# Optimization experiments

Hardware: AMD Instinct MI355X
Metric: run time of the kernel (lower is better)

## Reference

```python
import jax, jax.numpy as jnp
import numpy as np

TAU = 1.0
BASE = 7
NUM_TWISTS = 3
EPS = 1e-6

B, S, D, P, M = 4, 2048, 1024, 9, 256


def _rot(y, theta):
    # learned rotation in the (0,1) channel plane; theta broadcasts against y[..., 0]
    c, s = jnp.cos(theta), jnp.sin(theta)
    y0, y1 = y[..., 0], y[..., 1]
    r0 = (y0 * c - y1 * s)[..., None]
    r1 = (y0 * s + y1 * c)[..., None]
    return jnp.concatenate([r0, r1, y[..., 2:]], axis=-1)


def _mod_phase_norm(x, g, base=BASE):
    # RMS-normalize within channel groups defined by (channel index mod base)
    d = x.shape[-1]
    gid = jnp.arange(d) % base
    oh = jax.nn.one_hot(gid, base, dtype=x.dtype)           # [d, base]
    cnt = oh.sum(axis=0)                                    # [base]
    msq = (x * x) @ oh / cnt                                # [..., base]
    denom = jnp.sqrt(jnp.take(msq, gid, axis=-1) + EPS)     # [..., d]
    return x / denom * g


def setup_inputs() -> dict:
    key = jax.random.key(0)
    ks = jax.random.split(key, 16)
    w = lambda k, shape, scale: jax.random.normal(k, shape, dtype=jnp.float32) * scale
    u = jax.random.uniform(ks[1], (NUM_TWISTS + 1, B, S, P), dtype=jnp.float32,
                           minval=1e-6, maxval=1.0 - 1e-6)
    gumbel_noise = -jnp.log(-jnp.log(u))
    return {
        'x': w(ks[0], (B, S, D), 1.0),
        'gumbel_noise': gumbel_noise,
        'mixer_w': w(ks[2], (3, D), 0.5),
        'obs_W1': w(ks[3], (2 * D, M), (2 * D) ** -0.5),
        'obs_b1': jnp.zeros((M,), jnp.float32),
        'obs_th1': w(ks[4], (), 0.1),
        'obs_W2': w(ks[5], (M, P), M ** -0.5),
        'obs_b2': jnp.zeros((P,), jnp.float32),
        'obs_th2': w(ks[6], (), 0.1),
        'path_Wa': w(ks[7], (P, D, M), D ** -0.5),
        'path_ba': jnp.zeros((P, M), jnp.float32),
        'path_tha': w(ks[8], (P,), 0.1),
        'path_Wb': w(ks[9], (P, M, D), M ** -0.5),
        'path_bb': jnp.zeros((P, D), jnp.float32),
        'path_thb': w(ks[10], (P,), 0.1),
        'twist_W': w(ks[11], (D, D), D ** -0.5),
        'twist_b': jnp.zeros((D,), jnp.float32),
        'twist_th': w(ks[12], (), 0.1),
        'norm_g': jnp.ones((D,), jnp.float32),
    }


def reference(x, gumbel_noise, mixer_w, obs_W1, obs_b1, obs_th1, obs_W2, obs_b2,
              obs_th2, path_Wa, path_ba, path_tha, path_Wb, path_bb, path_thb,
              twist_W, twist_b, twist_th, norm_g):
    # neighbor mixer: per-channel 3-tap mix over sequence (zero-padded, non-causal)
    xp = jnp.pad(x, ((0, 0), (1, 1), (0, 0)))
    x_mixed = x * mixer_w[0] + xp[:, :-2] * mixer_w[1] + xp[:, 2:] * mixer_w[2]

    def observer_logits(collapsed):
        combined = jnp.concatenate([x_mixed, collapsed], axis=-1)      # [B,S,2D]
        h = jnp.tanh(_rot(combined @ obs_W1 + obs_b1, obs_th1))        # [B,S,M]
        return _rot(h @ obs_W2 + obs_b2, obs_th2)                      # [B,S,P]

    def path_outputs_fn(tin):
        h = _rot(jnp.einsum('bsd,pdm->bspm', tin, path_Wa) + path_ba, path_tha)
        return _rot(jnp.einsum('bspm,pmd->bspd', h, path_Wb) + path_bb, path_thb)

    collapsed = jnp.zeros_like(x_mixed)
    path_out = None
    for t in range(NUM_TWISTS):
        logits = observer_logits(collapsed)
        rw = jax.nn.softmax((logits + gumbel_noise[t]) / TAU, axis=-1)  # soft gumbel
        tin = x_mixed + _rot(collapsed @ twist_W + twist_b, twist_th)
        path_out = path_outputs_fn(tin)                                # [B,S,P,D]
        collapsed = _mod_phase_norm(jnp.einsum('bspd,bsp->bsd', path_out, rw), norm_g)

    # final hard (straight-through) gumbel routing, reusing last path_out
    final_logits = observer_logits(collapsed)
    soft = jax.nn.softmax((final_logits + gumbel_noise[NUM_TWISTS]) / TAU, axis=-1)
    hard = jax.nn.one_hot(jnp.argmax(soft, axis=-1), P, dtype=soft.dtype)
    rw_hard = hard + soft - jax.lax.stop_gradient(soft)
    final_collapsed = jnp.einsum('bspd,bsp->bsd', path_out, rw_hard)

    # dropout is identity in eval mode
    out = _mod_phase_norm(x + final_collapsed, norm_g)
    collapsed = _mod_phase_norm(collapsed, norm_g)
    return out, collapsed
```

## Files before the change

kernel.cpp:

```cpp
#include <hip/hip_runtime.h>
#include <hip/hip_bf16.h>

typedef unsigned short u16;
typedef short bf16x8 __attribute__((ext_vector_type(8)));
typedef float f32x4 __attribute__((ext_vector_type(4)));

constexpr int Dd = 1024, Pp = 9, Mm = 256, Nn = 8192, Kc = 2304;
constexpr float EPSf = 1e-6f;

__device__ __forceinline__ float bf2f(u16 u) {
    union { unsigned int u; float f; } v; v.u = ((unsigned int)u) << 16; return v.f;
}
__device__ __forceinline__ u16 f2bf(float f) {
    union { float f; unsigned int u; } v; v.f = f;
    unsigned int r = (v.u + 0x7FFFu + ((v.u >> 16) & 1u)) >> 16; return (u16)r;
}
__device__ __forceinline__ void split2(float v, u16& h, u16& l) {
    h = f2bf(v); l = f2bf(v - bf2f(h));
}
__device__ __forceinline__ void gld16(u16* lds, const u16* g) {
    __builtin_amdgcn_global_load_lds(
        (const __attribute__((address_space(1))) unsigned int*)g,
        (__attribute__((address_space(3))) unsigned int*)lds, 16, 0, 0);
}

__global__ void rotcopy_k(const float* __restrict__ src, float* __restrict__ dst,
                          int R, int C, const float* __restrict__ theta, int Pb)
{
    long total = (long)Pb * R * C;
    long idx = (long)blockIdx.x * 256 + threadIdx.x;
    if (idx >= total) return;
    int c = (int)(idx % C);
    long rp = idx / C;
    int r = (int)(rp % R);
    int pb = (int)(rp / R);
    float th = theta[pb];
    const float* s = src + ((long)pb * R + r) * C;
    float v;
    if (c == 0)      v = s[0] * cosf(th) - s[1] * sinf(th);
    else if (c == 1) v = s[0] * sinf(th) + s[1] * cosf(th);
    else             v = s[c];
    dst[idx] = v;
}

__global__ void splitW1_k(const float* __restrict__ W1, const float* __restrict__ th,
                          u16* __restrict__ h, u16* __restrict__ l)
{
    int idx = blockIdx.x * 256 + threadIdx.x;
    if (idx >= 256 * 2048) return;
    int k = idx & 2047, n = idx >> 11;
    float v;
    if (n == 0)      v = W1[(long)k * 256 + 0] * cosf(th[0]) - W1[(long)k * 256 + 1] * sinf(th[0]);
    else if (n == 1) v = W1[(long)k * 256 + 0] * sinf(th[0]) + W1[(long)k * 256 + 1] * cosf(th[0]);
    else             v = W1[(long)k * 256 + n];
    u16 hh, ll; split2(v, hh, ll); h[idx] = hh; l[idx] = ll;
}

__global__ void splitTW_k(const float* __restrict__ tW, const float* __restrict__ th,
                          u16* __restrict__ h, u16* __restrict__ l)
{
    int idx = blockIdx.x * 256 + threadIdx.x;
    if (idx >= 1024 * 1024) return;
    int k = idx & 1023, n = idx >> 10;
    float v;
    if (n == 0)      v = tW[(long)k * 1024 + 0] * cosf(th[0]) - tW[(long)k * 1024 + 1] * sinf(th[0]);
    else if (n == 1) v = tW[(long)k * 1024 + 0] * sinf(th[0]) + tW[(long)k * 1024 + 1] * cosf(th[0]);
    else             v = tW[(long)k * 1024 + n];
    u16 hh, ll; split2(v, hh, ll); h[idx] = hh; l[idx] = ll;
}

__global__ void splitWa_k(const float* __restrict__ Wa, const float* __restrict__ tha,
                          u16* __restrict__ h, u16* __restrict__ l)
{
    int idx = blockIdx.x * 256 + threadIdx.x;
    if (idx >= Kc * 1024) return;
    int k = idx & 1023, n = idx >> 10;
    int p = n >> 8, m = n & 255;
    const float* s = Wa + ((long)p * 1024 + k) * 256;
    float v;
    if (m == 0)      v = s[0] * cosf(tha[p]) - s[1] * sinf(tha[p]);
    else if (m == 1) v = s[0] * sinf(tha[p]) + s[1] * cosf(tha[p]);
    else             v = s[m];
    u16 hh, ll; split2(v, hh, ll); h[idx] = hh; l[idx] = ll;
}

__global__ void splitWb_k(const float* __restrict__ Wb, const float* __restrict__ thb,
                          u16* __restrict__ h, u16* __restrict__ l)
{
    int idx = blockIdx.x * 256 + threadIdx.x;
    if (idx >= 1024 * Kc) return;
    int n = idx / Kc;
    int k = idx - n * Kc;
    int p = k >> 8, m = k & 255;
    const float* s = Wb + ((long)p * 256 + m) * 1024;
    float v;
    if (n == 0)      v = s[0] * cosf(thb[p]) - s[1] * sinf(thb[p]);
    else if (n == 1) v = s[0] * sinf(thb[p]) + s[1] * cosf(thb[p]);
    else             v = s[n];
    u16 hh, ll; split2(v, hh, ll); h[idx] = hh; l[idx] = ll;
}

__global__ void mixer_k(const float* __restrict__ x, const float* __restrict__ mw,
                        u16* __restrict__ xmh, u16* __restrict__ xml)
{
    int idx = blockIdx.x * 256 + threadIdx.x;
    if (idx >= Nn * Dd / 4) return;
    int d4 = idx & (Dd / 4 - 1);
    int n = idx >> 8;
    int s = n & 2047;
    const float4* x4 = (const float4*)x;
    const float4* w4 = (const float4*)mw;
    float4 xc = x4[idx];
    float4 w0 = w4[d4], w1 = w4[(Dd / 4) + d4], w2 = w4[2 * (Dd / 4) + d4];
    float o[4];
    o[0] = xc.x * w0.x; o[1] = xc.y * w0.y; o[2] = xc.z * w0.z; o[3] = xc.w * w0.w;
    if (s > 0) {
        float4 xl = x4[idx - Dd / 4];
        o[0] += xl.x * w1.x; o[1] += xl.y * w1.y; o[2] += xl.z * w1.z; o[3] += xl.w * w1.w;
    }
    if (s < 2047) {
        float4 xr = x4[idx + Dd / 4];
        o[0] += xr.x * w2.x; o[1] += xr.y * w2.y; o[2] += xr.z * w2.z; o[3] += xr.w * w2.w;
    }
    ushort4 h4, l4;
    split2(o[0], h4.x, l4.x); split2(o[1], h4.y, l4.y);
    split2(o[2], h4.z, l4.z); split2(o[3], h4.w, l4.w);
    ((ushort4*)xmh)[idx] = h4; ((ushort4*)xml)[idx] = l4;
}

__global__ void tanh_k(const float* __restrict__ a, float* __restrict__ o, int total)
{
    int idx = blockIdx.x * 256 + threadIdx.x;
    if (idx < total) o[idx] = tanhf(a[idx]);
}

__global__ void addb_split_k(const u16* __restrict__ xmh, const u16* __restrict__ xml,
                             const float* __restrict__ tbr,
                             u16* __restrict__ th_, u16* __restrict__ tl_)
{
    int idx = blockIdx.x * 256 + threadIdx.x;
    if (idx >= Nn * Dd / 4) return;
    int d4 = idx & (Dd / 4 - 1);
    ushort4 xh = ((const ushort4*)xmh)[idx], xl = ((const ushort4*)xml)[idx];
    float4 b = ((const float4*)tbr)[d4];
    ushort4 h4, l4;
    split2(bf2f(xh.x) + bf2f(xl.x) + b.x, h4.x, l4.x);
    split2(bf2f(xh.y) + bf2f(xl.y) + b.y, h4.y, l4.y);
    split2(bf2f(xh.z) + bf2f(xl.z) + b.z, h4.z, l4.z);
    split2(bf2f(xh.w) + bf2f(xl.w) + b.w, h4.w, l4.w);
    ((ushort4*)th_)[idx] = h4; ((ushort4*)tl_)[idx] = l4;
}

template<int EPI>
__global__ __launch_bounds__(256, 2) void mgemm(
    const u16* __restrict__ Agh, const u16* __restrict__ Agl, int lda,
    const u16* __restrict__ Bgh, const u16* __restrict__ Bgl, int ldb,
    int K,
    float* __restrict__ Cf, u16* __restrict__ Coh, u16* __restrict__ Col, int ldc,
    const float* __restrict__ Cinit,
    const u16* __restrict__ CIh, const u16* __restrict__ CIl,
    const float* __restrict__ bias,
    const float* __restrict__ rwv,
    const float* __restrict__ rwv2,
    const float* __restrict__ bbrv)
{
    __shared__ u16 smem[2][16384];
    const int tid = threadIdx.x, wave = tid >> 6, lane = tid & 63;
    const int nwg = gridDim.x * gridDim.y;
    const int flat = blockIdx.y * gridDim.x + blockIdx.x;
    const int q = nwg >> 3;
    const int l_ = (flat & 7) * q + (flat >> 3);
    const int r0 = (l_ / gridDim.x) * 128, c0 = (l_ % gridDim.x) * 128;
    const int srl = lane >> 2;
    const int ssl = ((lane & 3) ^ ((lane >> 3) & 3)) * 8;
    const int frl = lane & 15, kh = lane >> 4;
    const int sw  = (kh ^ ((frl >> 1) & 3)) * 8;
    const int arow0 = (wave >> 1) * 64, bcol0 = (wave & 1) * 64;
    const int w32 = wave * 32;

    f32x4 acc[4][4] = {};
    f32x4 acc2[4][4];
    if constexpr (EPI == 4) {
#pragma unroll
        for (int i = 0; i < 4; ++i)
#pragma unroll
            for (int j = 0; j < 4; ++j) acc2[i][j] = f32x4{0.f, 0.f, 0.f, 0.f};
    }

    auto STAGE = [&](int buf, int k0) {
        u16* base = &smem[buf][0];
        u16* As_h = base;        u16* As_l = base + 4096;
        u16* Bs_h = base + 8192; u16* Bs_l = base + 12288;
        const long ga0 = (long)(r0 + w32 + srl) * lda + k0 + ssl;
        gld16(&As_h[w32 * 32],        Agh + ga0);
        gld16(&As_h[(w32 + 16) * 32], Agh + ga0 + 16L * lda);
        gld16(&As_l[w32 * 32],        Agl + ga0);
        gld16(&As_l[(w32 + 16) * 32], Agl + ga0 + 16L * lda);
        const long gb0 = (long)(c0 + w32 + srl) * ldb + k0 + ssl;
        gld16(&Bs_h[w32 * 32],        Bgh + gb0);
        gld16(&Bs_h[(w32 + 16) * 32], Bgh + gb0 + 16L * ldb);
        gld16(&Bs_l[w32 * 32],        Bgl + gb0);
        gld16(&Bs_l[(w32 + 16) * 32], Bgl + gb0 + 16L * ldb);
    };
    auto COMPUTE = [&](int buf, f32x4 (&ac)[4][4]) {
        u16* base = &smem[buf][0];
        u16* As_h = base;        u16* As_l = base + 4096;
        u16* Bs_h = base + 8192; u16* Bs_l = base + 12288;
        bf16x8 ah[4], al[4];
#pragma unroll
        for (int f = 0; f < 4; ++f) {
            int ao = (arow0 + f * 16 + frl) * 32 + sw;
            ah[f] = *(const bf16x8*)&As_h[ao];
            al[f] = *(const bf16x8*)&As_l[ao];
        }
#pragma unroll
        for (int j = 0; j < 4; ++j) {
            int bo = (bcol0 + j * 16 + frl) * 32 + sw;
            bf16x8 bh = *(const bf16x8*)&Bs_h[bo];
            bf16x8 bl = *(const bf16x8*)&Bs_l[bo];
#pragma unroll
            for (int i = 0; i < 4; ++i) {
                ac[i][j] = __builtin_amdgcn_mfma_f32_16x16x32_bf16(ah[i], bh, ac[i][j], 0, 0, 0);
                ac[i][j] = __builtin_amdgcn_mfma_f32_16x16x32_bf16(ah[i], bl, ac[i][j], 0, 0, 0);
                ac[i][j] = __builtin_amdgcn_mfma_f32_16x16x32_bf16(al[i], bh, ac[i][j], 0, 0, 0);
            }
        }
    };
    auto FLUSH = [&](int p) {
#pragma unroll
        for (int i = 0; i < 4; ++i)
#pragma unroll
            for (int reg = 0; reg < 4; ++reg) {
                float w = rwv[(long)(r0 + arow0 + i * 16 + kh * 4 + reg) * 9 + p];
#pragma unroll
                for (int j = 0; j < 4; ++j) {
                    acc[i][j][reg] += w * acc2[i][j][reg];
                    acc2[i][j][reg] = 0.f;
                }
            }
    };

    const int NT = K / 32;
    STAGE(0, 0);
#pragma unroll 1
    for (int t = 0; t < NT; t += 2) {
        STAGE(1, (t + 1) * 32);
        asm volatile("s_waitcnt vmcnt(8)" ::: "memory");
        __builtin_amdgcn_sched_barrier(0);
        __builtin_amdgcn_s_barrier();
        __builtin_amdgcn_sched_barrier(0);
        if constexpr (EPI == 4) COMPUTE(0, acc2); else COMPUTE(0, acc);
        __builtin_amdgcn_sched_barrier(0);
        __builtin_amdgcn_s_barrier();
        __builtin_amdgcn_sched_barrier(0);
        if (t + 2 < NT) {
            STAGE(0, (t + 2) * 32);
            asm volatile("s_waitcnt vmcnt(8)" ::: "memory");
        } else {
            asm volatile("s_waitcnt vmcnt(0)" ::: "memory");
        }
        __builtin_amdgcn_sched_barrier(0);
        __builtin_amdgcn_s_barrier();
        __builtin_amdgcn_sched_barrier(0);
        if constexpr (EPI == 4) COMPUTE(1, acc2); else COMPUTE(1, acc);
        __builtin_amdgcn_sched_barrier(0);
        __builtin_amdgcn_s_barrier();
        __builtin_amdgcn_sched_barrier(0);
        if constexpr (EPI == 4) {
            if (((t + 1) & 7) == 7) FLUSH((t + 1) >> 3);
        }
    }

#pragma unroll
    for (int i = 0; i < 4; ++i)
#pragma unroll
        for (int reg = 0; reg < 4; ++reg) {
            const int r = r0 + arow0 + i * 16 + kh * 4 + reg;
#pragma unroll
            for (int j = 0; j < 4; ++j) {
                const int c = c0 + bcol0 + j * 16 + frl;
                float v = acc[i][j][reg];
                if constexpr (EPI == 0) {
                    Cf[(long)r * ldc + c] = v + bias[c];
                } else if constexpr (EPI == 1) {
                    Cf[(long)r * ldc + c] = tanhf(v + Cinit[(long)r * ldc + c]);
                } else if constexpr (EPI == 2) {
                    long o = (long)r * ldc + c;
                    v += bf2f(CIh[o]) + bf2f(CIl[o]) + bias[c];
                    u16 h, l; split2(v, h, l); Coh[o] = h; Col[o] = l;
                } else if constexpr (EPI == 3) {
                    long o = (long)r * ldc + c;
                    v = (v + bias[c]) * rwv[(long)r * 9 + (c >> 8)];
                    u16 h, l; split2(v, h, l); Coh[o] = h; Col[o] = l;
                } else if constexpr (EPI == 4) {
#pragma unroll
                    for (int p = 0; p < 9; ++p) v += rwv2[(long)r * 9 + p] * bbrv[p * 1024 + c];
                    Cf[(long)r * ldc + c] = v;
                } else {
#pragma unroll
                    for (int p = 0; p < 9; ++p) v += rwv[(long)r * 9 + p] * bbrv[p * 1024 + c];
                    Cf[(long)r * ldc + c] = v;
                }
            }
        }
}

__global__ void logits_k(const float* __restrict__ h, const float* __restrict__ W2r,
                         const float* __restrict__ b2r, const float* __restrict__ gum,
                         float* __restrict__ rwA, float* __restrict__ rwH,
                         const float* __restrict__ rwS, int hard)
{
    __shared__ float hs[Mm];
    __shared__ float lg[16];
    int n = blockIdx.x;
    for (int i = threadIdx.x; i < Mm; i += 64) hs[i] = h[(long)n * Mm + i];
    __syncthreads();
    if (threadIdx.x < Pp) {
        int p = threadIdx.x;
        float acc = b2r[p];
        for (int m = 0; m < Mm; ++m) acc += hs[m] * W2r[m * Pp + p];
        lg[p] = acc + gum[(long)n * Pp + p];
    }
    __syncthreads();
    if (threadIdx.x == 0) {
        float mx = lg[0]; int am = 0;
#pragma unroll
        for (int p = 1; p < Pp; ++p) if (lg[p] > mx) { mx = lg[p]; am = p; }
        if (hard) {
#pragma unroll
            for (int p = 0; p < Pp; ++p) {
                rwA[(long)n * Pp + p] = (p == am) ? 1.f / rwS[(long)n * Pp + p] : 0.f;
                rwH[(long)n * Pp + p] = (p == am) ? 1.f : 0.f;
            }
        } else {
            float e[Pp]; float ssum = 0.f;
#pragma unroll
            for (int p = 0; p < Pp; ++p) { e[p] = expf(lg[p] - mx); ssum += e[p]; }
#pragma unroll
            for (int p = 0; p < Pp; ++p) rwA[(long)n * Pp + p] = e[p] / ssum;
        }
    }
}

template<int INSPLIT, int OUTSPLIT>
__global__ void norm_k(const float* __restrict__ in,
                       const u16* __restrict__ inh, const u16* __restrict__ inl,
                       const float* __restrict__ add, const float* __restrict__ g,
                       float* __restrict__ outf, u16* __restrict__ oh, u16* __restrict__ ol)
{
    __shared__ float sb[256][8];
    __shared__ float dn[8];
    int n = blockIdx.x;
    int t = threadIdx.x;
    float v[4];
#pragma unroll
    for (int j = 0; j < 7; ++j) sb[t][j] = 0.f;
#pragma unroll
    for (int i = 0; i < 4; ++i) {
        int d = t + i * 256;
        long o = (long)n * Dd + d;
        float xv = INSPLIT ? (bf2f(inh[o]) + bf2f(inl[o])) : in[o];
        if (add) xv += add[o];
        v[i] = xv;
        sb[t][d % 7] += xv * xv;
    }
    __syncthreads();
    for (int st = 128; st >= 1; st >>= 1) {
        if (t < st) {
#pragma unroll
            for (int j = 0; j < 7; ++j) sb[t][j] += sb[t + st][j];
        }
        __syncthreads();
    }
    if (t < 7) {
        const float cnt = (t < 2) ? 147.f : 146.f;
        dn[t] = 1.f / sqrtf(sb[0][t] / cnt + EPSf);
    }
    __syncthreads();
#pragma unroll
    for (int i = 0; i < 4; ++i) {
        int d = t + i * 256;
        long o = (long)n * Dd + d;
        float ov = v[i] * dn[d % 7] * g[d];
        if (OUTSPLIT) { u16 h, l; split2(ov, h, l); oh[o] = h; ol[o] = l; }
        else outf[o] = ov;
    }
}

static inline int cdiv(long a, long b) { return (int)((a + b - 1) / b); }

extern "C" void kernel_launch(void* const* d_in, const int* in_sizes, int n_in,
                              void* d_out, int out_size, void* d_ws, size_t ws_size,
                              hipStream_t stream)
{
    const float* x    = (const float*)d_in[0];
    const float* gum  = (const float*)d_in[1];
    const float* mw   = (const float*)d_in[2];
    const float* W1   = (const float*)d_in[3];
    const float* b1   = (const float*)d_in[4];
    const float* th1  = (const float*)d_in[5];
    const float* W2   = (const float*)d_in[6];
    const float* b2   = (const float*)d_in[7];
    const float* th2  = (const float*)d_in[8];
    const float* Wa   = (const float*)d_in[9];
    const float* ba   = (const float*)d_in[10];
    const float* tha  = (const float*)d_in[11];
    const float* Wb   = (const float*)d_in[12];
    const float* bbv  = (const float*)d_in[13];
    const float* thb  = (const float*)d_in[14];
    const float* tW   = (const float*)d_in[15];
    const float* tb   = (const float*)d_in[16];
    const float* tth  = (const float*)d_in[17];
    const float* gnorm = (const float*)d_in[18];

    char* cur = (char*)d_ws;
    auto alloc = [&](size_t bytes) -> void* {
        void* r = (void*)cur; cur += (bytes + 255) & ~(size_t)255; return r;
    };
    void* region = alloc((size_t)Nn * Dd * 4);
    float* craw = (float*)region;
    float* hbuf = (float*)region;
    u16*   tinh = (u16*)region;
    u16*   tinl = tinh + (size_t)Nn * Dd;
    float* zx   = (float*)alloc((size_t)Nn * Mm * 4);
    float* rwS  = (float*)alloc((size_t)Nn * Pp * 4);
    float* rwD  = (float*)alloc((size_t)Nn * Pp * 4);
    float* rwH  = (float*)alloc((size_t)Nn * Pp * 4);
    u16* xmh  = (u16*)alloc((size_t)Nn * Dd * 2);
    u16* xml  = (u16*)alloc((size_t)Nn * Dd * 2);
    u16* colh = (u16*)alloc((size_t)Nn * Dd * 2);
    u16* coll = (u16*)alloc((size_t)Nn * Dd * 2);
    u16* hph  = (u16*)alloc((size_t)Nn * Kc * 2);
    u16* hpl  = (u16*)alloc((size_t)Nn * Kc * 2);
    u16* W1th = (u16*)alloc(256 * 2048 * 2);
    u16* W1tl = (u16*)alloc(256 * 2048 * 2);
    u16* tWth = (u16*)alloc(1024 * 1024 * 2);
    u16* tWtl = (u16*)alloc(1024 * 1024 * 2);
    u16* Wath = (u16*)alloc((size_t)Kc * 1024 * 2);
    u16* Watl = (u16*)alloc((size_t)Kc * 1024 * 2);
    u16* Wbth = (u16*)alloc((size_t)1024 * Kc * 2);
    u16* Wbtl = (u16*)alloc((size_t)1024 * Kc * 2);
    float* W2r = (float*)alloc(256 * 9 * 4);
    float* b1r = (float*)alloc(256 * 4);
    float* b2r = (float*)alloc(16 * 4);
    float* bac = (float*)alloc(Kc * 4);
    float* bbr = (float*)alloc(Pp * 1024 * 4);
    float* tbr = (float*)alloc(1024 * 4);
    if ((size_t)(cur - (char*)d_ws) > ws_size) return;

    float* out0 = (float*)d_out;
    float* out1 = out0 + (long)Nn * Dd;

    splitW1_k<<<2048, 256, 0, stream>>>(W1, th1, W1th, W1tl);
    splitTW_k<<<4096, 256, 0, stream>>>(tW, tth, tWth, tWtl);
    splitWa_k<<<cdiv((long)Kc * 1024, 256), 256, 0, stream>>>(Wa, tha, Wath, Watl);
    splitWb_k<<<cdiv((long)1024 * Kc, 256), 256, 0, stream>>>(Wb, thb, Wbth, Wbtl);
    rotcopy_k<<<cdiv(256L * 9, 256), 256, 0, stream>>>(W2, W2r, 256, 9, th2, 1);
    rotcopy_k<<<1, 256, 0, stream>>>(b1, b1r, 1, 256, th1, 1);
    rotcopy_k<<<1, 256, 0, stream>>>(b2, b2r, 1, 9, th2, 1);
    rotcopy_k<<<cdiv((long)Pp * Mm, 256), 256, 0, stream>>>(ba, bac, 1, 256, tha, 9);
    rotcopy_k<<<cdiv((long)Pp * 1024, 256), 256, 0, stream>>>(bbv, bbr, 1, 1024, thb, 9);
    rotcopy_k<<<cdiv(1024L, 256), 256, 0, stream>>>(tb, tbr, 1, 1024, tth, 1);

    mixer_k<<<Nn * Dd / 4 / 256, 256, 0, stream>>>(x, mw, xmh, xml);

    mgemm<0><<<dim3(2, 64), 256, 0, stream>>>(
        xmh, xml, 1024, W1th, W1tl, 2048, 1024,
        zx, nullptr, nullptr, 256, nullptr, nullptr, nullptr, b1r, nullptr, nullptr, nullptr);

    for (int t = 0; t < 3; ++t) {
        if (t == 0) {
            tanh_k<<<cdiv((long)Nn * Mm, 256), 256, 0, stream>>>(zx, hbuf, Nn * Mm);
        } else {
            mgemm<1><<<dim3(2, 64), 256, 0, stream>>>(
                colh, coll, 1024, W1th + 1024, W1tl + 1024, 2048, 1024,
                hbuf, nullptr, nullptr, 256, zx, nullptr, nullptr, nullptr, nullptr, nullptr, nullptr);
        }
        logits_k<<<Nn, 64, 0, stream>>>(hbuf, W2r, b2r, gum + (long)t * Nn * Pp,
                                        rwS, nullptr, nullptr, 0);
        if (t == 0) {
            addb_split_k<<<Nn * Dd / 4 / 256, 256, 0, stream>>>(xmh, xml, tbr, tinh, tinl);
        } else {
            mgemm<2><<<dim3(8, 64), 256, 0, stream>>>(
                colh, coll, 1024, tWth, tWtl, 1024, 1024,
                nullptr, tinh, tinl, 1024, nullptr, xmh, xml, tbr, nullptr, nullptr, nullptr);
        }
        mgemm<3><<<dim3(18, 64), 256, 0, stream>>>(
            tinh, tinl, 1024, Wath, Watl, 1024, 1024,
            nullptr, hph, hpl, Kc, nullptr, nullptr, nullptr, bac, rwS, nullptr, nullptr);
        mgemm<5><<<dim3(8, 64), 256, 0, stream>>>(
            hph, hpl, Kc, Wbth, Wbtl, Kc, Kc,
            craw, nullptr, nullptr, 1024, nullptr, nullptr, nullptr, nullptr, rwS, nullptr, bbr);
        norm_k<0, 1><<<Nn, 256, 0, stream>>>(craw, nullptr, nullptr, nullptr, gnorm,
                                             nullptr, colh, coll);
    }

    mgemm<1><<<dim3(2, 64), 256, 0, stream>>>(
        colh, coll, 1024, W1th + 1024, W1tl + 1024, 2048, 1024,
        hbuf, nullptr, nullptr, 256, zx, nullptr, nullptr, nullptr, nullptr, nullptr, nullptr);
    logits_k<<<Nn, 64, 0, stream>>>(hbuf, W2r, b2r, gum + 3L * Nn * Pp,
                                    rwD, rwH, rwS, 1);
    mgemm<4><<<dim3(8, 64), 256, 0, stream>>>(
        hph, hpl, Kc, Wbth, Wbtl, Kc, Kc,
        craw, nullptr, nullptr, 1024, nullptr, nullptr, nullptr, nullptr, rwD, rwH, bbr);
    norm_k<0, 0><<<Nn, 256, 0, stream>>>(craw, nullptr, nullptr, x, gnorm, out0, nullptr, nullptr);
    norm_k<1, 0><<<Nn, 256, 0, stream>>>(nullptr, colh, coll, nullptr, gnorm, out1, nullptr, nullptr);
}
```

Measured before the change: 1.434 ms.

## Add 512-thread 256x128 tiled GEMM with register-prefetched B for big GEMMs

Adds a new mgemm2 kernel with 512 threads, a 256x128 output tile per workgroup, and an LDS double buffer for A. B fragments are loaded straight from global memory into registers one K-tile ahead, and MFMA sections run under raised priority. Workgroup ids are remapped so that neighbouring blocks share data in cache. The twist, path-A and path-B GEMMs move to this kernel to get more reuse per workgroup and better overlap of loads with MFMA, at the cost of more registers and fewer workgroups.

```diff
diff --git a/kernel.cpp b/kernel.cpp
--- a/kernel.cpp
+++ b/kernel.cpp
@@ -7,6 +7,8 @@
 
 constexpr int Dd = 1024, Pp = 9, Mm = 256, Nn = 8192, Kc = 2304;
 constexpr float EPSf = 1e-6f;
+
+template<int N> struct ic { static constexpr int v = N; };
 
 __device__ __forceinline__ float bf2f(u16 u) {
     union { unsigned int u; float f; } v; v.u = ((unsigned int)u) << 16; return v.f;
@@ -284,7 +286,113 @@
                     Cf[(long)r * ldc + c] = v + bias[c];
                 } else if constexpr (EPI == 1) {
                     Cf[(long)r * ldc + c] = tanhf(v + Cinit[(long)r * ldc + c]);
-                } else if constexpr (EPI == 2) {
+                } else if constexpr (EPI == 4) {
+#pragma unroll
+                    for (int p = 0; p < 9; ++p) v += rwv2[(long)r * 9 + p] * bbrv[p * 1024 + c];
+                    Cf[(long)r * ldc + c] = v;
+                }
+            }
+        }
+}
+
+template<int EPI>
+__global__ __launch_bounds__(512, 2) void mgemm2(
+    const u16* __restrict__ Agh, const u16* __restrict__ Agl, int lda,
+    const u16* __restrict__ Bgh, const u16* __restrict__ Bgl, int ldb,
+    int K,
+    float* __restrict__ Cf, u16* __restrict__ Coh, u16* __restrict__ Col, int ldc,
+    const u16* __restrict__ CIh, const u16* __restrict__ CIl,
+    const float* __restrict__ bias,
+    const float* __restrict__ rwv,
+    const float* __restrict__ bbrv)
+{
+    __shared__ u16 smem[2][16384];
+    const int tid = threadIdx.x, wave = tid >> 6, lane = tid & 63;
+    const int nwg = gridDim.x * gridDim.y;
+    const int flat = blockIdx.y * gridDim.x + blockIdx.x;
+    const int q = nwg >> 3;
+    const int l_ = (flat & 7) * q + (flat >> 3);
+    const int r0 = (l_ / gridDim.x) * 256, c0 = (l_ % gridDim.x) * 128;
+    const int srl = lane >> 2;
+    const int ssl = ((lane & 3) ^ ((lane >> 3) & 3)) * 8;
+    const int frl = lane & 15, kh = lane >> 4;
+    const int sw  = (kh ^ ((frl >> 1) & 3)) * 8;
+    const int arow0 = (wave >> 1) * 64, bcol0 = (wave & 1) * 64;
+    const int w32 = wave * 32;
+    const int NT = K / 32;
+
+    f32x4 acc[4][4] = {};
+    bf16x8 bA[8], bB[8];
+
+    auto STAGE_A = [&](int buf, int k0) {
+        u16* Ash = &smem[buf][0];
+        u16* Asl = &smem[buf][8192];
+        const long ga = (long)(r0 + w32 + srl) * lda + k0 + ssl;
+        gld16(&Ash[w32 * 32],        Agh + ga);
+        gld16(&Ash[(w32 + 16) * 32], Agh + ga + 16L * lda);
+        gld16(&Asl[w32 * 32],        Agl + ga);
+        gld16(&Asl[(w32 + 16) * 32], Agl + ga + 16L * lda);
+    };
+    auto LOADB1 = [&](bf16x8 (&dst)[8], int j, int k0) {
+        const long gb = (long)(c0 + bcol0 + j * 16 + frl) * ldb + k0 + kh * 8;
+        dst[j * 2]     = *(const bf16x8*)(Bgh + gb);
+        dst[j * 2 + 1] = *(const bf16x8*)(Bgl + gb);
+    };
+
+    auto TILE = [&](auto P, int t, bf16x8 (&bcur)[8], bf16x8 (&bnxt)[8]) {
+        constexpr int par = decltype(P)::v;
+        asm volatile("s_waitcnt vmcnt(0) lgkmcnt(0)" ::: "memory");
+        __builtin_amdgcn_sched_barrier(0);
+        __builtin_amdgcn_s_barrier();
+        __builtin_amdgcn_sched_barrier(0);
+        if (t + 1 < NT) STAGE_A(par ^ 1, (t + 1) * 32);
+        u16* Ash = &smem[par][0];
+        u16* Asl = &smem[par][8192];
+        bf16x8 ah[4], al[4];
+#pragma unroll
+        for (int f = 0; f < 4; ++f) {
+            int ao = (arow0 + f * 16 + frl) * 32 + sw;
+            ah[f] = *(const bf16x8*)&Ash[ao];
+            al[f] = *(const bf16x8*)&Asl[ao];
+        }
+#pragma unroll
+        for (int j = 0; j < 4; ++j) {
+            bf16x8 bh = bcur[j * 2], bl = bcur[j * 2 + 1];
+            __builtin_amdgcn_s_setprio(1);
+#pragma unroll
+            for (int i = 0; i < 4; ++i)
+                acc[i][j] = __builtin_amdgcn_mfma_f32_16x16x32_bf16(ah[i], bh, acc[i][j], 0, 0, 0);
+#pragma unroll
+            for (int i = 0; i < 4; ++i)
+                acc[i][j] = __builtin_amdgcn_mfma_f32_16x16x32_bf16(ah[i], bl, acc[i][j], 0, 0, 0);
+#pragma unroll
+            for (int i = 0; i < 4; ++i)
+                acc[i][j] = __builtin_amdgcn_mfma_f32_16x16x32_bf16(al[i], bh, acc[i][j], 0, 0, 0);
+            __builtin_amdgcn_s_setprio(0);
+            if (t + 1 < NT) LOADB1(bnxt, j, (t + 1) * 32);
+        }
+    };
+
+    STAGE_A(0, 0);
+#pragma unroll
+    for (int j = 0; j < 4; ++j) LOADB1(bA, j, 0);
+
+#pragma unroll 1
+    for (int t = 0; t < NT; t += 2) {
+        TILE(ic<0>{}, t,     bA, bB);
+        TILE(ic<1>{}, t + 1, bB, bA);
+    }
+
+#pragma unroll
+    for (int i = 0; i < 4; ++i)
+#pragma unroll
+        for (int reg = 0; reg < 4; ++reg) {
+            const int r = r0 + arow0 + i * 16 + kh * 4 + reg;
+#pragma unroll
+            for (int j = 0; j < 4; ++j) {
+                const int c = c0 + bcol0 + j * 16 + frl;
+                float v = acc[i][j][reg];
+                if constexpr (EPI == 2) {
                     long o = (long)r * ldc + c;
                     v += bf2f(CIh[o]) + bf2f(CIl[o]) + bias[c];
                     u16 h, l; split2(v, h, l); Coh[o] = h; Col[o] = l;
@@ -292,10 +400,6 @@
                     long o = (long)r * ldc + c;
                     v = (v + bias[c]) * rwv[(long)r * 9 + (c >> 8)];
                     u16 h, l; split2(v, h, l); Coh[o] = h; Col[o] = l;
-                } else if constexpr (EPI == 4) {
-#pragma unroll
-                    for (int p = 0; p < 9; ++p) v += rwv2[(long)r * 9 + p] * bbrv[p * 1024 + c];
-                    Cf[(long)r * ldc + c] = v;
                 } else {
 #pragma unroll
                     for (int p = 0; p < 9; ++p) v += rwv[(long)r * 9 + p] * bbrv[p * 1024 + c];
@@ -481,16 +585,16 @@
         if (t == 0) {
             addb_split_k<<<Nn * Dd / 4 / 256, 256, 0, stream>>>(xmh, xml, tbr, tinh, tinl);
         } else {
-            mgemm<2><<<dim3(8, 64), 256, 0, stream>>>(
+            mgemm2<2><<<dim3(8, 32), 512, 0, stream>>>(
                 colh, coll, 1024, tWth, tWtl, 1024, 1024,
-                nullptr, tinh, tinl, 1024, nullptr, xmh, xml, tbr, nullptr, nullptr, nullptr);
-        }
-        mgemm<3><<<dim3(18, 64), 256, 0, stream>>>(
+                nullptr, tinh, tinl, 1024, xmh, xml, tbr, nullptr, nullptr);
+        }
+        mgemm2<3><<<dim3(18, 32), 512, 0, stream>>>(
             tinh, tinl, 1024, Wath, Watl, 1024, 1024,
-            nullptr, hph, hpl, Kc, nullptr, nullptr, nullptr, bac, rwS, nullptr, nullptr);
-        mgemm<5><<<dim3(8, 64), 256, 0, stream>>>(
+            nullptr, hph, hpl, Kc, nullptr, nullptr, bac, rwS, nullptr);
+        mgemm2<5><<<dim3(8, 32), 512, 0, stream>>>(
             hph, hpl, Kc, Wbth, Wbtl, Kc, Kc,
-            craw, nullptr, nullptr, 1024, nullptr, nullptr, nullptr, nullptr, rwS, nullptr, bbr);
+            craw, nullptr, nullptr, 1024, nullptr, nullptr, nullptr, rwS, bbr);
         norm_k<0, 1><<<Nn, 256, 0, stream>>>(craw, nullptr, nullptr, nullptr, gnorm,
                                              nullptr, colh, coll);
     }
```

Measured after the change: 2.109 ms. 47.1% more time.

## Fold twist matrix into path-A weights to skip per-iteration twist GEMM

Applied to the files above, without the earlier changes.

Precomputes a fused weight (twist_W rotated, times path_Wa) and a fused bias, so each later iteration computes hidden path activations straight from collapsed with one GEMM plus a precomputed x_mixed@Wa term. This removes the 1024x1024 twist GEMM and the tin intermediate per iteration. The first iteration uses an elementwise kernel on the precomputed x_mixed projection. It costs one extra Nn x Kc split buffer and a weight-product GEMM at setup, and falls back to the old path if workspace is too small. Pre-multiplying the weights changes the rounding order of the split-bf16 arithmetic.

```diff
diff --git a/kernel.cpp b/kernel.cpp
--- a/kernel.cpp
+++ b/kernel.cpp
@@ -69,6 +69,20 @@
     u16 hh, ll; split2(v, hh, ll); h[idx] = hh; l[idx] = ll;
 }
 
+__global__ void splitTWT_k(const float* __restrict__ tW, const float* __restrict__ th,
+                           u16* __restrict__ h, u16* __restrict__ l)
+{
+    int idx = blockIdx.x * 256 + threadIdx.x;
+    if (idx >= 1024 * 1024) return;
+    int d = idx & 1023, e = idx >> 10;
+    const float* s = tW + (long)e * 1024;
+    float v;
+    if (d == 0)      v = s[0] * cosf(th[0]) - s[1] * sinf(th[0]);
+    else if (d == 1) v = s[0] * sinf(th[0]) + s[1] * cosf(th[0]);
+    else             v = s[d];
+    u16 hh, ll; split2(v, hh, ll); h[idx] = hh; l[idx] = ll;
+}
+
 __global__ void splitWa_k(const float* __restrict__ Wa, const float* __restrict__ tha,
                           u16* __restrict__ h, u16* __restrict__ l)
 {
@@ -98,6 +112,44 @@
     else if (n == 1) v = s[0] * sinf(thb[p]) + s[1] * cosf(thb[p]);
     else             v = s[n];
     u16 hh, ll; split2(v, hh, ll); h[idx] = hh; l[idx] = ll;
+}
+
+__global__ void bac2_k(const float* __restrict__ bac, const float* __restrict__ tbr,
+                       const u16* __restrict__ Wath, const u16* __restrict__ Watl,
+                       float* __restrict__ bac2)
+{
+    __shared__ float sb[256];
+    int pm = blockIdx.x;
+    int t = threadIdx.x;
+    float s = 0.f;
+    for (int d = t; d < 1024; d += 256) {
+        long o = (long)pm * 1024 + d;
+        s += tbr[d] * (bf2f(Wath[o]) + bf2f(Watl[o]));
+    }
+    sb[t] = s; __syncthreads();
+    for (int st = 128; st >= 1; st >>= 1) {
+        if (t < st) sb[t] += sb[t + st];
+        __syncthreads();
+    }
+    if (t == 0) bac2[pm] = bac[pm] + sb[0];
+}
+
+__global__ void hp0_k(const u16* __restrict__ zxah, const u16* __restrict__ zxal,
+                      const float* __restrict__ rw,
+                      u16* __restrict__ hph, u16* __restrict__ hpl)
+{
+    int idx = blockIdx.x * 256 + threadIdx.x;
+    if (idx >= Nn * Kc / 4) return;
+    int c4 = idx % (Kc / 4);
+    int n  = idx / (Kc / 4);
+    float w = rw[(long)n * Pp + (c4 >> 6)];
+    ushort4 zh = ((const ushort4*)zxah)[idx], zl = ((const ushort4*)zxal)[idx];
+    ushort4 h4, l4;
+    split2((bf2f(zh.x) + bf2f(zl.x)) * w, h4.x, l4.x);
+    split2((bf2f(zh.y) + bf2f(zl.y)) * w, h4.y, l4.y);
+    split2((bf2f(zh.z) + bf2f(zl.z)) * w, h4.z, l4.z);
+    split2((bf2f(zh.w) + bf2f(zl.w)) * w, h4.w, l4.w);
+    ((ushort4*)hph)[idx] = h4; ((ushort4*)hpl)[idx] = l4;
 }
 
 __global__ void mixer_k(const float* __restrict__ x, const float* __restrict__ mw,
@@ -279,27 +331,32 @@
 #pragma unroll
             for (int j = 0; j < 4; ++j) {
                 const int c = c0 + bcol0 + j * 16 + frl;
+                const long o = (long)r * ldc + c;
                 float v = acc[i][j][reg];
                 if constexpr (EPI == 0) {
-                    Cf[(long)r * ldc + c] = v + bias[c];
+                    Cf[o] = v + bias[c];
                 } else if constexpr (EPI == 1) {
-                    Cf[(long)r * ldc + c] = tanhf(v + Cinit[(long)r * ldc + c]);
+                    Cf[o] = tanhf(v + Cinit[o]);
                 } else if constexpr (EPI == 2) {
-                    long o = (long)r * ldc + c;
                     v += bf2f(CIh[o]) + bf2f(CIl[o]) + bias[c];
                     u16 h, l; split2(v, h, l); Coh[o] = h; Col[o] = l;
                 } else if constexpr (EPI == 3) {
-                    long o = (long)r * ldc + c;
                     v = (v + bias[c]) * rwv[(long)r * 9 + (c >> 8)];
                     u16 h, l; split2(v, h, l); Coh[o] = h; Col[o] = l;
                 } else if constexpr (EPI == 4) {
 #pragma unroll
                     for (int p = 0; p < 9; ++p) v += rwv2[(long)r * 9 + p] * bbrv[p * 1024 + c];
-                    Cf[(long)r * ldc + c] = v;
+                    Cf[o] = v;
+                } else if constexpr (EPI == 5) {
+#pragma unroll
+                    for (int p = 0; p < 9; ++p) v += rwv[(long)r * 9 + p] * bbrv[p * 1024 + c];
+                    Cf[o] = v;
+                } else if constexpr (EPI == 6) {
+                    if (bias) v += bias[c];
+                    u16 h, l; split2(v, h, l); Coh[o] = h; Col[o] = l;
                 } else {
-#pragma unroll
-                    for (int p = 0; p < 9; ++p) v += rwv[(long)r * 9 + p] * bbrv[p * 1024 + c];
-                    Cf[(long)r * ldc + c] = v;
+                    v = (v + bf2f(CIh[o]) + bf2f(CIl[o])) * rwv[(long)r * 9 + (c >> 8)];
+                    u16 h, l; split2(v, h, l); Coh[o] = h; Col[o] = l;
                 }
             }
         }
@@ -388,6 +445,7 @@
 }
 
 static inline int cdiv(long a, long b) { return (int)((a + b - 1) / b); }
+static inline size_t al256(size_t b) { return (b + 255) & ~(size_t)255; }
 
 extern "C" void kernel_launch(void* const* d_in, const int* in_sizes, int n_in,
                               void* d_out, int out_size, void* d_ws, size_t ws_size,
@@ -413,46 +471,56 @@
     const float* tth  = (const float*)d_in[17];
     const float* gnorm = (const float*)d_in[18];
 
+    const size_t szRegion = al256((size_t)Nn * Dd * 4);
+    const size_t szZx   = al256((size_t)Nn * Mm * 4);
+    const size_t szRw   = al256((size_t)Nn * Pp * 4);
+    const size_t szColH = al256((size_t)Nn * Dd * 2);
+    const size_t szHpH  = al256((size_t)Nn * Kc * 2);
+    const size_t szW1H  = al256((size_t)256 * 2048 * 2);
+    const size_t szWatH = al256((size_t)Kc * 1024 * 2);
+    const size_t szWbH  = al256((size_t)1024 * Kc * 2);
+    const size_t szTWH  = al256((size_t)1024 * 1024 * 2);
+    const size_t szMisc = al256(256 * 9 * 4) + al256(256 * 4) + al256(64)
+                        + al256(Kc * 4) + al256(Kc * 4) + al256(Pp * 1024 * 4) + al256(1024 * 4);
+    const size_t need_common = szRegion + szZx + 3 * szRw + 2 * szColH + 2 * szHpH
+                             + 2 * szW1H + 2 * szWatH + 2 * szWbH + szMisc;
+    const size_t need_new = 2 * szHpH  + 2 * szTWH  + 2 * szWatH ;
+    const size_t need_old = 2 * szColH  + 2 * szTWH ;
+    const bool NEWP = ws_size >= need_common + need_new;
+    if (!NEWP && ws_size < need_common + need_old) return;
+
     char* cur = (char*)d_ws;
-    auto alloc = [&](size_t bytes) -> void* {
-        void* r = (void*)cur; cur += (bytes + 255) & ~(size_t)255; return r;
-    };
+    auto alloc = [&](size_t bytes) -> void* { void* r = cur; cur += al256(bytes); return r; };
+
     void* region = alloc((size_t)Nn * Dd * 4);
-    float* craw = (float*)region;
-    float* hbuf = (float*)region;
-    u16*   tinh = (u16*)region;
-    u16*   tinl = tinh + (size_t)Nn * Dd;
     float* zx   = (float*)alloc((size_t)Nn * Mm * 4);
     float* rwS  = (float*)alloc((size_t)Nn * Pp * 4);
     float* rwD  = (float*)alloc((size_t)Nn * Pp * 4);
     float* rwH  = (float*)alloc((size_t)Nn * Pp * 4);
-    u16* xmh  = (u16*)alloc((size_t)Nn * Dd * 2);
-    u16* xml  = (u16*)alloc((size_t)Nn * Dd * 2);
     u16* colh = (u16*)alloc((size_t)Nn * Dd * 2);
     u16* coll = (u16*)alloc((size_t)Nn * Dd * 2);
     u16* hph  = (u16*)alloc((size_t)Nn * Kc * 2);
     u16* hpl  = (u16*)alloc((size_t)Nn * Kc * 2);
     u16* W1th = (u16*)alloc(256 * 2048 * 2);
     u16* W1tl = (u16*)alloc(256 * 2048 * 2);
-    u16* tWth = (u16*)alloc(1024 * 1024 * 2);
-    u16* tWtl = (u16*)alloc(1024 * 1024 * 2);
     u16* Wath = (u16*)alloc((size_t)Kc * 1024 * 2);
     u16* Watl = (u16*)alloc((size_t)Kc * 1024 * 2);
     u16* Wbth = (u16*)alloc((size_t)1024 * Kc * 2);
     u16* Wbtl = (u16*)alloc((size_t)1024 * Kc * 2);
-    float* W2r = (float*)alloc(256 * 9 * 4);
-    float* b1r = (float*)alloc(256 * 4);
-    float* b2r = (float*)alloc(16 * 4);
-    float* bac = (float*)alloc(Kc * 4);
-    float* bbr = (float*)alloc(Pp * 1024 * 4);
-    float* tbr = (float*)alloc(1024 * 4);
-    if ((size_t)(cur - (char*)d_ws) > ws_size) return;
-
+    float* W2r  = (float*)alloc(256 * 9 * 4);
+    float* b1r  = (float*)alloc(256 * 4);
+    float* b2r  = (float*)alloc(64);
+    float* bac  = (float*)alloc(Kc * 4);
+    float* bac2 = (float*)alloc(Kc * 4);
+    float* bbr  = (float*)alloc(Pp * 1024 * 4);
+    float* tbr  = (float*)alloc(1024 * 4);
+
+    float* hbuf = (float*)region;
+    float* craw = (float*)region;
     float* out0 = (float*)d_out;
     float* out1 = out0 + (long)Nn * Dd;
 
     splitW1_k<<<2048, 256, 0, stream>>>(W1, th1, W1th, W1tl);
-    splitTW_k<<<4096, 256, 0, stream>>>(tW, tth, tWth, tWtl);
     splitWa_k<<<cdiv((long)Kc * 1024, 256), 256, 0, stream>>>(Wa, tha, Wath, Watl);
     splitWb_k<<<cdiv((long)1024 * Kc, 256), 256, 0, stream>>>(Wb, thb, Wbth, Wbtl);
     rotcopy_k<<<cdiv(256L * 9, 256), 256, 0, stream>>>(W2, W2r, 256, 9, th2, 1);
@@ -462,47 +530,125 @@
     rotcopy_k<<<cdiv((long)Pp * 1024, 256), 256, 0, stream>>>(bbv, bbr, 1, 1024, thb, 9);
     rotcopy_k<<<cdiv(1024L, 256), 256, 0, stream>>>(tb, tbr, 1, 1024, tth, 1);
 
-    mixer_k<<<Nn * Dd / 4 / 256, 256, 0, stream>>>(x, mw, xmh, xml);
-
-    mgemm<0><<<dim3(2, 64), 256, 0, stream>>>(
-        xmh, xml, 1024, W1th, W1tl, 2048, 1024,
-        zx, nullptr, nullptr, 256, nullptr, nullptr, nullptr, b1r, nullptr, nullptr, nullptr);
-
-    for (int t = 0; t < 3; ++t) {
-        if (t == 0) {
-            tanh_k<<<cdiv((long)Nn * Mm, 256), 256, 0, stream>>>(zx, hbuf, Nn * Mm);
-        } else {
-            mgemm<1><<<dim3(2, 64), 256, 0, stream>>>(
-                colh, coll, 1024, W1th + 1024, W1tl + 1024, 2048, 1024,
-                hbuf, nullptr, nullptr, 256, zx, nullptr, nullptr, nullptr, nullptr, nullptr, nullptr);
-        }
-        logits_k<<<Nn, 64, 0, stream>>>(hbuf, W2r, b2r, gum + (long)t * Nn * Pp,
-                                        rwS, nullptr, nullptr, 0);
-        if (t == 0) {
-            addb_split_k<<<Nn * Dd / 4 / 256, 256, 0, stream>>>(xmh, xml, tbr, tinh, tinl);
-        } else {
-            mgemm<2><<<dim3(8, 64), 256, 0, stream>>>(
-                colh, coll, 1024, tWth, tWtl, 1024, 1024,
-                nullptr, tinh, tinl, 1024, nullptr, xmh, xml, tbr, nullptr, nullptr, nullptr);
-        }
-        mgemm<3><<<dim3(18, 64), 256, 0, stream>>>(
-            tinh, tinl, 1024, Wath, Watl, 1024, 1024,
-            nullptr, hph, hpl, Kc, nullptr, nullptr, nullptr, bac, rwS, nullptr, nullptr);
-        mgemm<5><<<dim3(8, 64), 256, 0, stream>>>(
+    if (NEWP) {
+        u16* zxah  = (u16*)alloc((size_t)Nn * Kc * 2);
+        u16* zxal  = (u16*)alloc((size_t)Nn * Kc * 2);
+        u16* tWtTh = (u16*)alloc((size_t)1024 * 1024 * 2);
+        u16* tWtTl = (u16*)alloc((size_t)1024 * 1024 * 2);
+        u16* Wfath = (u16*)alloc((size_t)Kc * 1024 * 2);
+        u16* Wfatl = (u16*)alloc((size_t)Kc * 1024 * 2);
+        u16* xmh = (u16*)region;
+        u16* xml = xmh + (size_t)Nn * Dd;
+
+        splitTWT_k<<<4096, 256, 0, stream>>>(tW, tth, tWtTh, tWtTl);
+        mgemm<6><<<dim3(8, 18), 256, 0, stream>>>(
+            Wath, Watl, 1024, tWtTh, tWtTl, 1024, 1024,
+            nullptr, Wfath, Wfatl, 1024, nullptr, nullptr, nullptr,
+            nullptr, nullptr, nullptr, nullptr);
+        bac2_k<<<Kc, 256, 0, stream>>>(bac, tbr, Wath, Watl, bac2);
+
+        mixer_k<<<Nn * Dd / 4 / 256, 256, 0, stream>>>(x, mw, xmh, xml);
+        mgemm<0><<<dim3(2, 64), 256, 0, stream>>>(
+            xmh, xml, 1024, W1th, W1tl, 2048, 1024,
+            zx, nullptr, nullptr, 256, nullptr, nullptr, nullptr,
+            b1r, nullptr, nullptr, nullptr);
+        mgemm<6><<<dim3(18, 64), 256, 0, stream>>>(
+            xmh, xml, 1024, Wath, Watl, 1024, 1024,
+            nullptr, zxah, zxal, Kc, nullptr, nullptr, nullptr,
+            bac2, nullptr, nullptr, nullptr);
+
+        for (int t = 0; t < 3; ++t) {
+            if (t == 0) {
+                tanh_k<<<cdiv((long)Nn * Mm, 256), 256, 0, stream>>>(zx, hbuf, Nn * Mm);
+            } else {
+                mgemm<1><<<dim3(2, 64), 256, 0, stream>>>(
+                    colh, coll, 1024, W1th + 1024, W1tl + 1024, 2048, 1024,
+                    hbuf, nullptr, nullptr, 256, zx, nullptr, nullptr,
+                    nullptr, nullptr, nullptr, nullptr);
+            }
+            logits_k<<<Nn, 64, 0, stream>>>(hbuf, W2r, b2r, gum + (long)t * Nn * Pp,
+                                            rwS, nullptr, nullptr, 0);
+            if (t == 0) {
+                hp0_k<<<cdiv((long)Nn * Kc / 4, 256), 256, 0, stream>>>(zxah, zxal, rwS, hph, hpl);
+            } else {
+                mgemm<7><<<dim3(18, 64), 256, 0, stream>>>(
+                    colh, coll, 1024, Wfath, Wfatl, 1024, 1024,
+                    nullptr, hph, hpl, Kc, nullptr, zxah, zxal,
+                    nullptr, rwS, nullptr, nullptr);
+            }
+            mgemm<5><<<dim3(8, 64), 256, 0, stream>>>(
+                hph, hpl, Kc, Wbth, Wbtl, Kc, Kc,
+                craw, nullptr, nullptr, 1024, nullptr, nullptr, nullptr,
+                nullptr, rwS, nullptr, bbr);
+            norm_k<0, 1><<<Nn, 256, 0, stream>>>(craw, nullptr, nullptr, nullptr, gnorm,
+                                                 nullptr, colh, coll);
+        }
+        mgemm<1><<<dim3(2, 64), 256, 0, stream>>>(
+            colh, coll, 1024, W1th + 1024, W1tl + 1024, 2048, 1024,
+            hbuf, nullptr, nullptr, 256, zx, nullptr, nullptr,
+            nullptr, nullptr, nullptr, nullptr);
+        logits_k<<<Nn, 64, 0, stream>>>(hbuf, W2r, b2r, gum + 3L * Nn * Pp, rwD, rwH, rwS, 1);
+        mgemm<4><<<dim3(8, 64), 256, 0, stream>>>(
             hph, hpl, Kc, Wbth, Wbtl, Kc, Kc,
-            craw, nullptr, nullptr, 1024, nullptr, nullptr, nullptr, nullptr, rwS, nullptr, bbr);
-        norm_k<0, 1><<<Nn, 256, 0, stream>>>(craw, nullptr, nullptr, nullptr, gnorm,
-                                             nullptr, colh, coll);
-    }
-
-    mgemm<1><<<dim3(2, 64), 256, 0, stream>>>(
-        colh, coll, 1024, W1th + 1024, W1tl + 1024, 2048, 1024,
-        hbuf, nullptr, nullptr, 256, zx, nullptr, nullptr, nullptr, nullptr, nullptr, nullptr);
-    logits_k<<<Nn, 64, 0, stream>>>(hbuf, W2r, b2r, gum + 3L * Nn * Pp,
-                                    rwD, rwH, rwS, 1);
-    mgemm<4><<<dim3(8, 64), 256, 0, stream>>>(
-        hph, hpl, Kc, Wbth, Wbtl, Kc, Kc,
-        craw, nullptr, nullptr, 1024, nullptr, nullptr, nullptr, nullptr, rwD, rwH, bbr);
-    norm_k<0, 0><<<Nn, 256, 0, stream>>>(craw, nullptr, nullptr, x, gnorm, out0, nullptr, nullptr);
-    norm_k<1, 0><<<Nn, 256, 0, stream>>>(nullptr, colh, coll, nullptr, gnorm, out1, nullptr, nullptr);
-}
+            craw, nullptr, nullptr, 1024, nullptr, nullptr, nullptr,
+            nullptr, rwD, rwH, bbr);
+        norm_k<0, 0><<<Nn, 256, 0, stream>>>(craw, nullptr, nullptr, x, gnorm, out0, nullptr, nullptr);
+        norm_k<1, 0><<<Nn, 256, 0, stream>>>(nullptr, colh, coll, nullptr, gnorm, out1, nullptr, nullptr);
+    } else {
+        u16* xmh  = (u16*)alloc((size_t)Nn * Dd * 2);
+        u16* xml  = (u16*)alloc((size_t)Nn * Dd * 2);
+        u16* tWth = (u16*)alloc((size_t)1024 * 1024 * 2);
+        u16* tWtl = (u16*)alloc((size_t)1024 * 1024 * 2);
+        u16* tinh = (u16*)region;
+        u16* tinl = tinh + (size_t)Nn * Dd;
+
+        splitTW_k<<<4096, 256, 0, stream>>>(tW, tth, tWth, tWtl);
+        mixer_k<<<Nn * Dd / 4 / 256, 256, 0, stream>>>(x, mw, xmh, xml);
+        mgemm<0><<<dim3(2, 64), 256, 0, stream>>>(
+            xmh, xml, 1024, W1th, W1tl, 2048, 1024,
+            zx, nullptr, nullptr, 256, nullptr, nullptr, nullptr,
+            b1r, nullptr, nullptr, nullptr);
+
+        for (int t = 0; t < 3; ++t) {
+            if (t == 0) {
+                tanh_k<<<cdiv((long)Nn * Mm, 256), 256, 0, stream>>>(zx, hbuf, Nn * Mm);
+            } else {
+                mgemm<1><<<dim3(2, 64), 256, 0, stream>>>(
+                    colh, coll, 1024, W1th + 1024, W1tl + 1024, 2048, 1024,
+                    hbuf, nullptr, nullptr, 256, zx, nullptr, nullptr,
+                    nullptr, nullptr, nullptr, nullptr);
+            }
+            logits_k<<<Nn, 64, 0, stream>>>(hbuf, W2r, b2r, gum + (long)t * Nn * Pp,
+                                            rwS, nullptr, nullptr, 0);
+            if (t == 0) {
+                addb_split_k<<<Nn * Dd / 4 / 256, 256, 0, stream>>>(xmh, xml, tbr, tinh, tinl);
+            } else {
+                mgemm<2><<<dim3(8, 64), 256, 0, stream>>>(
+                    colh, coll, 1024, tWth, tWtl, 1024, 1024,
+                    nullptr, tinh, tinl, 1024, nullptr, xmh, xml,
+                    tbr, nullptr, nullptr, nullptr);
+            }
+            mgemm<3><<<dim3(18, 64), 256, 0, stream>>>(
+                tinh, tinl, 1024, Wath, Watl, 1024, 1024,
+                nullptr, hph, hpl, Kc, nullptr, nullptr, nullptr,
+                bac, rwS, nullptr, nullptr);
+            mgemm<5><<<dim3(8, 64), 256, 0, stream>>>(
+                hph, hpl, Kc, Wbth, Wbtl, Kc, Kc,
+                craw, nullptr, nullptr, 1024, nullptr, nullptr, nullptr,
+                nullptr, rwS, nullptr, bbr);
+            norm_k<0, 1><<<Nn, 256, 0, stream>>>(craw, nullptr, nullptr, nullptr, gnorm,
+                                                 nullptr, colh, coll);
+        }
+        mgemm<1><<<dim3(2, 64), 256, 0, stream>>>(
+            colh, coll, 1024, W1th + 1024, W1tl + 1024, 2048, 1024,
+            hbuf, nullptr, nullptr, 256, zx, nullptr, nullptr,
+            nullptr, nullptr, nullptr, nullptr);
+        logits_k<<<Nn, 64, 0, stream>>>(hbuf, W2r, b2r, gum + 3L * Nn * Pp, rwD, rwH, rwS, 1);
+        mgemm<4><<<dim3(8, 64), 256, 0, stream>>>(
+            hph, hpl, Kc, Wbth, Wbtl, Kc, Kc,
+            craw, nullptr, nullptr, 1024, nullptr, nullptr, nullptr,
+            nullptr, rwD, rwH, bbr);
+        norm_k<0, 0><<<Nn, 256, 0, stream>>>(craw, nullptr, nullptr, x, gnorm, out0, nullptr, nullptr);
+        norm_k<1, 0><<<Nn, 256, 0, stream>>>(nullptr, colh, coll, nullptr, gnorm, out1, nullptr, nullptr);
+    }
+}
```

New measurement: 1.410 ms. About the same (-1.7%).
